# Kernel optimization log

Measured on AMD Instinct MI355X. Metric: run time of the kernel, lower is better.

## Reference

```python
import jax, jax.numpy as jnp
import numpy as np

D_MODEL = 1024
N_HEADS = 16
HEAD_DIM = D_MODEL // N_HEADS
N_MEM = 16
EPS = 1e-5
ROPE_THETA = 10000.0


def layernorm(x, g, b):
    mu = jnp.mean(x, axis=-1, keepdims=True)
    var = jnp.mean(jnp.square(x - mu), axis=-1, keepdims=True)
    return (x - mu) * jax.lax.rsqrt(var + EPS) * g + b


def rope_cos_sin(seq_len, head_dim, dtype):
    inv_freq = 1.0 / (ROPE_THETA ** (jnp.arange(0, head_dim, 2, dtype=jnp.float32) / head_dim))
    pos = jnp.arange(seq_len, dtype=jnp.float32)
    freqs = pos[:, None] * inv_freq[None, :]            # [S, hd/2]
    emb = jnp.concatenate([freqs, freqs], axis=-1)       # [S, hd]
    return jnp.cos(emb).astype(dtype), jnp.sin(emb).astype(dtype)


def rotate_half(x):
    x1, x2 = jnp.split(x, 2, axis=-1)
    return jnp.concatenate([-x2, x1], axis=-1)


def setup_inputs() -> dict:
    key = jax.random.key(0)
    ks = jax.random.split(key, 8)
    B, T, D = 2, 2048, D_MODEL
    x = jax.random.normal(ks[0], (B, T, D), dtype=jnp.float32)
    memory_tokens = jax.random.normal(ks[1], (1, N_MEM, D), dtype=jnp.float32) * 0.02
    s = 1.0 / np.sqrt(D)
    qkv_w = jax.random.uniform(ks[2], (3 * D, D), minval=-s, maxval=s, dtype=jnp.float32)
    qkv_b = jax.random.uniform(ks[3], (3 * D,), minval=-s, maxval=s, dtype=jnp.float32)
    out_w = jax.random.uniform(ks[4], (D, D), minval=-s, maxval=s, dtype=jnp.float32)
    out_b = jax.random.uniform(ks[5], (D,), minval=-s, maxval=s, dtype=jnp.float32)
    norm_g = jnp.ones((D,), jnp.float32)
    norm_b = jnp.zeros((D,), jnp.float32)
    normm_g = jnp.ones((D,), jnp.float32)
    normm_b = jnp.zeros((D,), jnp.float32)
    return {"x": x, "memory_tokens": memory_tokens, "qkv_w": qkv_w, "qkv_b": qkv_b,
            "out_w": out_w, "out_b": out_b, "norm_g": norm_g, "norm_b": norm_b,
            "normm_g": normm_g, "normm_b": normm_b}


def reference(x, memory_tokens, qkv_w, qkv_b, out_w, out_b, norm_g, norm_b, normm_g, normm_b):
    B, T, D = x.shape
    S = N_MEM + T
    residual = x
    x_norm = layernorm(x, norm_g, norm_b)
    mem = layernorm(jnp.broadcast_to(memory_tokens, (B, N_MEM, D)), normm_g, normm_b)
    xm = jnp.concatenate([mem, x_norm], axis=1)                # [B, S, D]
    qkv = xm @ qkv_w.T + qkv_b                                 # [B, S, 3D]
    qkv = qkv.reshape(B, S, 3, N_HEADS, HEAD_DIM)
    q = jnp.transpose(qkv[:, :, 0], (0, 2, 1, 3))              # [B, H, S, hd]
    k = jnp.transpose(qkv[:, :, 1], (0, 2, 1, 3))
    v = jnp.transpose(qkv[:, :, 2], (0, 2, 1, 3))
    cos, sin = rope_cos_sin(S, HEAD_DIM, x.dtype)              # [S, hd]
    q = q * cos + rotate_half(q) * sin
    k = k * cos + rotate_half(k) * sin
    scale = 1.0 / np.sqrt(HEAD_DIM)
    scores = jnp.einsum("bhqd,bhkd->bhqk", q, k) * scale       # [B, H, S, S]
    causal = jnp.tril(jnp.ones((S, S), dtype=bool))
    scores = jnp.where(causal, scores, jnp.finfo(scores.dtype).min)
    attn = jax.nn.softmax(scores, axis=-1)
    out = jnp.einsum("bhqk,bhkd->bhqd", attn, v)               # [B, H, S, hd]
    out = jnp.transpose(out, (0, 2, 1, 3)).reshape(B, S, D)
    out = out @ out_w.T + out_b
    out = out[:, N_MEM:, :]
    return residual + out
```

## Files before the change

### kernel.cpp

```cpp
#include <hip/hip_runtime.h>
#include <cstdint>


using bf16 = __bf16;
typedef __attribute__((ext_vector_type(8))) __bf16 bf16x8;
typedef __attribute__((ext_vector_type(4))) __bf16 bf16x4;
typedef __attribute__((ext_vector_type(4))) float floatx4;

#define MFMA16(a, b, c) __builtin_amdgcn_mfma_f32_16x16x32_bf16(a, b, c, 0, 0, 0)

constexpr int SV = 2064;
constexpr int SP = 2112;
constexpr float LOG2_THETA = 13.287712379549449f;

__device__ __forceinline__ bool dt_is_bf16(const void* p) {
  return *(const uint32_t*)p == 0x3F803F80u;
}

struct f8 { float v[8]; };

__device__ __forceinline__ f8 load8(const void* p, size_t idx, bool bf) {
  f8 r;
  if (bf) {
    bf16x8 t = *(const bf16x8*)((const bf16*)p + idx);
#pragma unroll
    for (int j = 0; j < 8; ++j) r.v[j] = (float)t[j];
  } else {
    float4 a = *(const float4*)((const float*)p + idx);
    float4 b = *(const float4*)((const float*)p + idx + 4);
    r.v[0] = a.x; r.v[1] = a.y; r.v[2] = a.z; r.v[3] = a.w;
    r.v[4] = b.x; r.v[5] = b.y; r.v[6] = b.z; r.v[7] = b.w;
  }
  return r;
}

__device__ __forceinline__ float ld1(const void* p, size_t idx, bool bf) {
  return bf ? (float)((const bf16*)p)[idx] : ((const float*)p)[idx];
}

__device__ __forceinline__ void load16_to_lds(const bf16* gptr, bf16* lptr) {
  auto* g = reinterpret_cast<const __attribute__((address_space(1))) uint32_t*>(
      reinterpret_cast<uintptr_t>(gptr));
  auto* l = reinterpret_cast<__attribute__((address_space(3))) uint32_t*>(
      reinterpret_cast<uintptr_t>(lptr));
  __builtin_amdgcn_global_load_lds(g, l, 16, 0, 0);
}

__global__ __launch_bounds__(256) void conv_w(
    const void* __restrict__ Wq, const void* __restrict__ Wo,
    const void* __restrict__ flagp, bf16* __restrict__ Wqb,
    bf16* __restrict__ Wob) {
  const bool bf = dt_is_bf16(flagp);
  const size_t i = ((size_t)blockIdx.x * 256 + threadIdx.x) * 8;
  const void* src;
  bf16* dst;
  size_t off;
  if (i < 3145728) { src = Wq; dst = Wqb; off = i; }
  else { src = Wo; dst = Wob; off = i - 3145728; }
  const f8 v = load8(src, off, bf);
  bf16x8 o;
#pragma unroll
  for (int j = 0; j < 8; ++j) o[j] = (bf16)v.v[j];
  *(bf16x8*)&dst[off] = o;
}

__global__ __launch_bounds__(256) void ln_all(
    const void* __restrict__ x, const void* __restrict__ mem,
    const void* __restrict__ ng, const void* __restrict__ nb,
    const void* __restrict__ mg, const void* __restrict__ mb,
    bf16* __restrict__ mem16, bf16* __restrict__ xln) {
  const bool bf = dt_is_bf16(ng);
  const int t = threadIdx.x, wid = t >> 6, lane = t & 63;
  const int row = blockIdx.x * 4 + wid;
  const void *src, *g, *bb;
  size_t soff;
  bf16* out;
  if (row < 16) {
    src = mem; soff = (size_t)row * 1024; g = mg; bb = mb;
    out = mem16 + (size_t)row * 1024;
  } else {
    src = x; soff = (size_t)(row - 16) * 1024; g = ng; bb = nb;
    out = xln + (size_t)(row - 16) * 1024;
  }
  const f8 v0 = load8(src, soff + lane * 8, bf);
  const f8 v1 = load8(src, soff + 512 + lane * 8, bf);
  float sum = 0.f, sq = 0.f;
#pragma unroll
  for (int j = 0; j < 8; ++j) { sum += v0.v[j]; sq += v0.v[j] * v0.v[j]; }
#pragma unroll
  for (int j = 0; j < 8; ++j) { sum += v1.v[j]; sq += v1.v[j] * v1.v[j]; }
#pragma unroll
  for (int off = 1; off < 64; off <<= 1) {
    sum += __shfl_xor(sum, off);
    sq += __shfl_xor(sq, off);
  }
  const float mu = sum * (1.0f / 1024.0f);
  const float var = sq * (1.0f / 1024.0f) - mu * mu;
  const float rstd = rsqrtf(var + 1e-5f);
  const f8 g0 = load8(g, lane * 8, bf), g1 = load8(g, 512 + lane * 8, bf);
  const f8 b0 = load8(bb, lane * 8, bf), b1 = load8(bb, 512 + lane * 8, bf);
  bf16x8 o0, o1;
#pragma unroll
  for (int j = 0; j < 8; ++j) {
    o0[j] = (bf16)((v0.v[j] - mu) * rstd * g0.v[j] + b0.v[j]);
    o1[j] = (bf16)((v1.v[j] - mu) * rstd * g1.v[j] + b1.v[j]);
  }
  *(bf16x8*)&out[lane * 8] = o0;
  *(bf16x8*)&out[512 + lane * 8] = o1;
}

__global__ __launch_bounds__(256) void gemm0_rope(
    const bf16* __restrict__ mem16, const bf16* __restrict__ xln,
    const bf16* __restrict__ Wqb, const void* __restrict__ bias,
    const void* __restrict__ flagp, bf16* __restrict__ Qg,
    bf16* __restrict__ Kg, bf16* __restrict__ Vg) {
  const bool bf = dt_is_bf16(flagp);
  __shared__ bf16 As[128 * 32];
  __shared__ bf16 Bs[128 * 32];
  const int t = threadIdx.x;
  const int row0 = blockIdx.x * 128;
  const int col0 = blockIdx.y * 128;
  const int wid = t >> 6, lane = t & 63, lr = lane & 15, lg = lane >> 4;
  const int wrow = (wid >> 1) * 64, wcol = (wid & 1) * 64;
  floatx4 acc[4][4] = {};

  const bf16* agp[2];
  const bf16* bgp[2];
#pragma unroll
  for (int c = 0; c < 2; ++c) {
    const int tt = c * 256 + t;
    int g = row0 + (tt >> 2);
    if (g > 4127) g = 4127;
    const int b2 = (g >= SV) ? 1 : 0;
    const int s = g - b2 * SV;
    const bf16* ap = (s < 16) ? (mem16 + (size_t)s * 1024)
                              : (xln + ((size_t)(b2 * 2048 + s - 16)) * 1024);
    agp[c] = ap + (tt & 3) * 8;
    bgp[c] = Wqb + (size_t)(col0 + (tt >> 2)) * 1024 + (tt & 3) * 8;
  }

  for (int k0 = 0; k0 < 1024; k0 += 32) {
    __syncthreads();
#pragma unroll
    for (int c = 0; c < 2; ++c) {
      const int tt = c * 256 + t;
      load16_to_lds(agp[c] + k0, &As[(tt & ~63) * 8]);
      load16_to_lds(bgp[c] + k0, &Bs[(tt & ~63) * 8]);
    }
    __syncthreads();
    bf16x8 af[4], bfr[4];
#pragma unroll
    for (int i = 0; i < 4; ++i) {
      af[i] = *(const bf16x8*)&As[(wrow + i * 16 + lr) * 32 + lg * 8];
      bfr[i] = *(const bf16x8*)&Bs[(wcol + i * 16 + lr) * 32 + lg * 8];
    }
#pragma unroll
    for (int mi = 0; mi < 4; ++mi)
#pragma unroll
      for (int ni = 0; ni < 4; ++ni)
        acc[mi][ni] = MFMA16(af[mi], bfr[ni], acc[mi][ni]);
  }

  const int colbase = col0 + wcol;
  const int part = colbase >> 10;
  const int h = (colbase >> 6) & 15;
  float f01[2];
  f01[0] = exp2f((float)lr * (-LOG2_THETA / 32.0f));
  f01[1] = exp2f((float)(16 + lr) * (-LOG2_THETA / 32.0f));

  if (part == 2) {
#pragma unroll
    for (int mi = 0; mi < 4; ++mi) {
      const int gq = row0 + wrow + mi * 16 + lg * 4;
      if (gq >= 2 * SV) continue;
      const int b2 = (gq >= SV) ? 1 : 0;
      const int pos = gq - b2 * SV;
      const size_t hb = (size_t)(b2 * 16 + h) * 64;
#pragma unroll
      for (int ni = 0; ni < 4; ++ni) {
        const int d = ni * 16 + lr;
        const float bc = ld1(bias, colbase + ni * 16 + lr, bf);
        bf16x4 vv;
#pragma unroll
        for (int r = 0; r < 4; ++r) vv[r] = (bf16)(acc[mi][ni][r] + bc);
        *(bf16x4*)&Vg[(hb + d) * SP + pos] = vv;
      }
    }
  } else {
    bf16* Dst = (part == 0) ? Qg : Kg;
    const float qs = (part == 0) ? 0.125f : 1.0f;
#pragma unroll
    for (int mi = 0; mi < 4; ++mi) {
#pragma unroll
      for (int r = 0; r < 4; ++r) {
        const int g = row0 + wrow + mi * 16 + lg * 4 + r;
        if (g >= 2 * SV) continue;
        const int b2 = (g >= SV) ? 1 : 0;
        const int pos = g - b2 * SV;
        bf16* drow = Dst + ((size_t)(b2 * 16 + h) * SP + pos) * 64;
#pragma unroll
        for (int a = 0; a < 2; ++a) {
          float c, sn;
          sincosf((float)pos * f01[a], &c, &sn);
          const float vlo = (acc[mi][a][r] + ld1(bias, colbase + a * 16 + lr, bf)) * qs;
          const float vhi = (acc[mi][a + 2][r] + ld1(bias, colbase + 32 + a * 16 + lr, bf)) * qs;
          drow[a * 16 + lr] = (bf16)(vlo * c - vhi * sn);
          drow[32 + a * 16 + lr] = (bf16)(vhi * c + vlo * sn);
        }
      }
    }
  }
}

__global__ __launch_bounds__(256) void flash3(
    const bf16* __restrict__ Qg, const bf16* __restrict__ Kg,
    const bf16* __restrict__ Vg, bf16* __restrict__ attn_out) {
  const int qt = 32 - blockIdx.x;
  const int bh = blockIdx.y;
  const int b = bh >> 4, h = bh & 15;
  const bf16* Qb = Qg + (size_t)bh * SP * 64;
  const bf16* Kb = Kg + (size_t)bh * SP * 64;
  const bf16* Vb = Vg + (size_t)bh * 64 * SP;

  const int t = threadIdx.x;
  const int wid = t >> 6, lane = t & 63, lr = lane & 15, lg = lane >> 4;
  const int qw0 = qt * 64 + wid * 16;

  __shared__ bf16 Ks[64 * 72];
  __shared__ bf16 Vt[64 * 64];
  __shared__ bf16 Ps[4][16 * 72];

  const int qs = qw0 + lr;
  bf16x8 qf0{}, qf1{};
  if (qs < SV) {
    qf0 = *(const bf16x8*)&Qb[(size_t)qs * 64 + lg * 8];
    qf1 = *(const bf16x8*)&Qb[(size_t)qs * 64 + 32 + lg * 8];
  }

  floatx4 o[4] = {};
  float lpart[4] = {};

  const int kr = t >> 2;
  const int kc = (t & 3) * 16;
  const int vd = t >> 2;
  const int vg0 = t & 3;
  const int vswz = ((vd & 7) ^ ((vd >> 4) & 3)) << 3;

  bf16x8 kA, kB, vA, vB;
  kA = *(const bf16x8*)&Kb[(size_t)kr * 64 + kc];
  kB = *(const bf16x8*)&Kb[(size_t)kr * 64 + kc + 8];
  vA = *(const bf16x8*)&Vb[(size_t)vd * SP + vg0 * 8];
  vB = *(const bf16x8*)&Vb[(size_t)vd * SP + (vg0 + 4) * 8];

  for (int kt = 0; kt <= qt; ++kt) {
    const int k0 = kt * 64;
    __syncthreads();
    *(bf16x8*)&Ks[kr * 72 + kc] = kA;
    *(bf16x8*)&Ks[kr * 72 + kc + 8] = kB;
    *(bf16x8*)&Vt[vd * 64 + ((vg0 << 3) ^ vswz)] = vA;
    *(bf16x8*)&Vt[vd * 64 + (((vg0 + 4) << 3) ^ vswz)] = vB;
    __syncthreads();
    if (kt < qt) {
      const int kn = k0 + 64;
      kA = *(const bf16x8*)&Kb[(size_t)(kn + kr) * 64 + kc];
      kB = *(const bf16x8*)&Kb[(size_t)(kn + kr) * 64 + kc + 8];
      vA = *(const bf16x8*)&Vb[(size_t)vd * SP + kn + vg0 * 8];
      vB = *(const bf16x8*)&Vb[(size_t)vd * SP + kn + (vg0 + 4) * 8];
    }

    floatx4 c[4] = {};
#pragma unroll
    for (int j2 = 0; j2 < 4; ++j2) {
      const bf16x8 kfa = *(const bf16x8*)&Ks[(j2 * 16 + lr) * 72 + lg * 8];
      const bf16x8 kfb = *(const bf16x8*)&Ks[(j2 * 16 + lr) * 72 + 32 + lg * 8];
      c[j2] = MFMA16(qf0, kfa, c[j2]);
      c[j2] = MFMA16(qf1, kfb, c[j2]);
    }

    const bool nm = (k0 + 63 > qw0);
#pragma unroll
    for (int r = 0; r < 4; ++r) {
      const int row = qw0 + lg * 4 + r;
      bf16* psr = &Ps[wid][(lg * 4 + r) * 72];
      float ls = 0.f;
#pragma unroll
      for (int j2 = 0; j2 < 4; ++j2) {
        float s = c[j2][r];
        if (nm && (k0 + j2 * 16 + lr > row)) s = -1e30f;
        const float p = __expf(s);
        ls += p;
        psr[j2 * 16 + lr] = (bf16)p;
      }
      lpart[r] += ls;
    }
    asm volatile("s_waitcnt lgkmcnt(0)" ::: "memory");
#pragma unroll
    for (int cc = 0; cc < 2; ++cc) {
      const bf16x8 pf = *(const bf16x8*)&Ps[wid][lr * 72 + cc * 32 + lg * 8];
#pragma unroll
      for (int dt = 0; dt < 4; ++dt) {
        const int key8 = (cc * 32 + lg * 8) ^ ((((lr & 7) ^ dt)) << 3);
        const bf16x8 vf = *(const bf16x8*)&Vt[(dt * 16 + lr) * 64 + key8];
        o[dt] = MFMA16(pf, vf, o[dt]);
      }
    }
  }

#pragma unroll
  for (int r = 0; r < 4; ++r) {
    float l = lpart[r];
    l += __shfl_xor(l, 1);
    l += __shfl_xor(l, 2);
    l += __shfl_xor(l, 4);
    l += __shfl_xor(l, 8);
    const int s = qw0 + lg * 4 + r;
    if (s < 16 || s >= SV) continue;
    const float inv = 1.0f / l;
    const size_t rowoff = ((size_t)(b * 2048 + s - 16)) * 1024 + h * 64;
#pragma unroll
    for (int dt = 0; dt < 4; ++dt)
      attn_out[rowoff + dt * 16 + lr] = (bf16)(o[dt][r] * inv);
  }
}

__global__ __launch_bounds__(256) void gemm1_proj(
    const bf16* __restrict__ A, const bf16* __restrict__ Wob,
    const void* __restrict__ bias, const void* __restrict__ x,
    const void* __restrict__ flagp, void* __restrict__ outp) {
  const bool bf = dt_is_bf16(flagp);
  __shared__ bf16 As[128 * 32];
  __shared__ bf16 Bs[128 * 32];
  const int t = threadIdx.x;
  const int row0 = blockIdx.x * 128;
  const int col0 = blockIdx.y * 128;
  const int wid = t >> 6, lane = t & 63, lr = lane & 15, lg = lane >> 4;
  const int wrow = (wid >> 1) * 64, wcol = (wid & 1) * 64;
  floatx4 acc[4][4] = {};

  const bf16* agp[2];
  const bf16* bgp[2];
#pragma unroll
  for (int c = 0; c < 2; ++c) {
    const int tt = c * 256 + t;
    agp[c] = A + (size_t)(row0 + (tt >> 2)) * 1024 + (tt & 3) * 8;
    bgp[c] = Wob + (size_t)(col0 + (tt >> 2)) * 1024 + (tt & 3) * 8;
  }

  for (int k0 = 0; k0 < 1024; k0 += 32) {
    __syncthreads();
#pragma unroll
    for (int c = 0; c < 2; ++c) {
      const int tt = c * 256 + t;
      load16_to_lds(agp[c] + k0, &As[(tt & ~63) * 8]);
      load16_to_lds(bgp[c] + k0, &Bs[(tt & ~63) * 8]);
    }
    __syncthreads();
    bf16x8 af[4], bfr[4];
#pragma unroll
    for (int i = 0; i < 4; ++i) {
      af[i] = *(const bf16x8*)&As[(wrow + i * 16 + lr) * 32 + lg * 8];
      bfr[i] = *(const bf16x8*)&Bs[(wcol + i * 16 + lr) * 32 + lg * 8];
    }
#pragma unroll
    for (int mi = 0; mi < 4; ++mi)
#pragma unroll
      for (int ni = 0; ni < 4; ++ni)
        acc[mi][ni] = MFMA16(af[mi], bfr[ni], acc[mi][ni]);
  }

#pragma unroll
  for (int mi = 0; mi < 4; ++mi) {
#pragma unroll
    for (int r = 0; r < 4; ++r) {
      const int row = row0 + wrow + mi * 16 + lg * 4 + r;
#pragma unroll
      for (int ni = 0; ni < 4; ++ni) {
        const int col = col0 + wcol + ni * 16 + lr;
        const size_t idx = (size_t)row * 1024 + col;
        const float v = acc[mi][ni][r] + ld1(bias, col, bf) + ld1(x, idx, bf);
        if (bf)
          ((bf16*)outp)[idx] = (bf16)v;
        else
          ((float*)outp)[idx] = v;
      }
    }
  }
}

extern "C" void kernel_launch(void* const* d_in, const int* in_sizes, int n_in,
                              void* d_out, int out_size, void* d_ws, size_t ws_size,
                              hipStream_t stream) {
  const void* x = d_in[0];
  const void* mem = d_in[1];
  const void* qkvw = d_in[2];
  const void* qkvb = d_in[3];
  const void* outw = d_in[4];
  const void* outb = d_in[5];
  const void* ng = d_in[6];
  const void* nb = d_in[7];
  const void* mg = d_in[8];
  const void* mb = d_in[9];

  char* ws = (char*)d_ws;
  bf16* mem16 = (bf16*)(ws);
  bf16* xln = (bf16*)(ws + 32768);
  bf16* Qg = (bf16*)(ws + 8421376);
  bf16* Kg = (bf16*)(ws + 17072128);
  bf16* Vg = (bf16*)(ws + 25722880);
  bf16* Wqb = (bf16*)(ws + 34373632);
  bf16* Wob = (bf16*)(ws + 40665088);
  bf16* attn = xln;

  conv_w<<<2048, 256, 0, stream>>>(qkvw, outw, ng, Wqb, Wob);
  ln_all<<<1028, 256, 0, stream>>>(x, mem, ng, nb, mg, mb, mem16, xln);
  gemm0_rope<<<dim3(33, 24), 256, 0, stream>>>(mem16, xln, Wqb, qkvb, ng,
                                               Qg, Kg, Vg);
  flash3<<<dim3(33, 32), 256, 0, stream>>>(Qg, Kg, Vg, attn);
  gemm1_proj<<<dim3(32, 8), 256, 0, stream>>>(attn, Wob, outb, x, ng, d_out);
}
```

Measured before the change: 240.8 us.

## Double attention query tile per block and merge weight-convert with layernorm

The flash attention kernel now gives each wave two 16-row query sub-tiles (a 128-row block), so every K/V tile staged in shared memory serves twice as many queries and grid size is halved. Sub-tiles fully above the causal diagonal skip work, and K/V loads past the padded end are clamped or zeroed. The weight conversion and layernorm kernels are fused into one launch to save launch overhead. The cost is more registers per thread and fewer blocks, which can lower occupancy and worsen load balance for the causal triangle.

```diff
diff --git a/kernel.cpp b/kernel.cpp
--- a/kernel.cpp
+++ b/kernel.cpp
@@ -46,32 +46,31 @@
   __builtin_amdgcn_global_load_lds(g, l, 16, 0, 0);
 }
 
-__global__ __launch_bounds__(256) void conv_w(
-    const void* __restrict__ Wq, const void* __restrict__ Wo,
-    const void* __restrict__ flagp, bf16* __restrict__ Wqb,
-    bf16* __restrict__ Wob) {
-  const bool bf = dt_is_bf16(flagp);
-  const size_t i = ((size_t)blockIdx.x * 256 + threadIdx.x) * 8;
-  const void* src;
-  bf16* dst;
-  size_t off;
-  if (i < 3145728) { src = Wq; dst = Wqb; off = i; }
-  else { src = Wo; dst = Wob; off = i - 3145728; }
-  const f8 v = load8(src, off, bf);
-  bf16x8 o;
-#pragma unroll
-  for (int j = 0; j < 8; ++j) o[j] = (bf16)v.v[j];
-  *(bf16x8*)&dst[off] = o;
-}
-
-__global__ __launch_bounds__(256) void ln_all(
+__global__ __launch_bounds__(256) void prep(
     const void* __restrict__ x, const void* __restrict__ mem,
     const void* __restrict__ ng, const void* __restrict__ nb,
     const void* __restrict__ mg, const void* __restrict__ mb,
-    bf16* __restrict__ mem16, bf16* __restrict__ xln) {
+    const void* __restrict__ Wq, const void* __restrict__ Wo,
+    bf16* __restrict__ mem16, bf16* __restrict__ xln,
+    bf16* __restrict__ Wqb, bf16* __restrict__ Wob) {
   const bool bf = dt_is_bf16(ng);
-  const int t = threadIdx.x, wid = t >> 6, lane = t & 63;
-  const int row = blockIdx.x * 4 + wid;
+  const int t = threadIdx.x;
+  if (blockIdx.x < 2048) {
+    const size_t i = ((size_t)blockIdx.x * 256 + t) * 8;
+    const void* src;
+    bf16* dst;
+    size_t off;
+    if (i < 3145728) { src = Wq; dst = Wqb; off = i; }
+    else { src = Wo; dst = Wob; off = i - 3145728; }
+    const f8 v = load8(src, off, bf);
+    bf16x8 o;
+#pragma unroll
+    for (int j = 0; j < 8; ++j) o[j] = (bf16)v.v[j];
+    *(bf16x8*)&dst[off] = o;
+    return;
+  }
+  const int wid = t >> 6, lane = t & 63;
+  const int row = (blockIdx.x - 2048) * 4 + wid;
   const void *src, *g, *bb;
   size_t soff;
   bf16* out;
@@ -212,10 +211,10 @@
   }
 }
 
-__global__ __launch_bounds__(256) void flash3(
+__global__ __launch_bounds__(256) void flash4(
     const bf16* __restrict__ Qg, const bf16* __restrict__ Kg,
     const bf16* __restrict__ Vg, bf16* __restrict__ attn_out) {
-  const int qt = 32 - blockIdx.x;
+  const int qt = 16 - blockIdx.x;
   const int bh = blockIdx.y;
   const int b = bh >> 4, h = bh & 15;
   const bf16* Qb = Qg + (size_t)bh * SP * 64;
@@ -224,21 +223,25 @@
 
   const int t = threadIdx.x;
   const int wid = t >> 6, lane = t & 63, lr = lane & 15, lg = lane >> 4;
-  const int qw0 = qt * 64 + wid * 16;
+  const int qw0 = qt * 128 + wid * 32;
 
   __shared__ bf16 Ks[64 * 72];
   __shared__ bf16 Vt[64 * 64];
-  __shared__ bf16 Ps[4][16 * 72];
-
-  const int qs = qw0 + lr;
-  bf16x8 qf0{}, qf1{};
-  if (qs < SV) {
-    qf0 = *(const bf16x8*)&Qb[(size_t)qs * 64 + lg * 8];
-    qf1 = *(const bf16x8*)&Qb[(size_t)qs * 64 + 32 + lg * 8];
-  }
-
-  floatx4 o[4] = {};
-  float lpart[4] = {};
+  __shared__ bf16 Ps[4][32 * 72];
+
+  const int qsa = qw0 + lr, qsb = qw0 + 16 + lr;
+  bf16x8 qa0{}, qa1{}, qb0{}, qb1{};
+  if (qsa < SV) {
+    qa0 = *(const bf16x8*)&Qb[(size_t)qsa * 64 + lg * 8];
+    qa1 = *(const bf16x8*)&Qb[(size_t)qsa * 64 + 32 + lg * 8];
+  }
+  if (qsb < SV) {
+    qb0 = *(const bf16x8*)&Qb[(size_t)qsb * 64 + lg * 8];
+    qb1 = *(const bf16x8*)&Qb[(size_t)qsb * 64 + 32 + lg * 8];
+  }
+
+  floatx4 oa[4] = {}, ob[4] = {};
+  float la[4] = {}, lb[4] = {};
 
   const int kr = t >> 2;
   const int kc = (t & 3) * 16;
@@ -246,13 +249,17 @@
   const int vg0 = t & 3;
   const int vswz = ((vd & 7) ^ ((vd >> 4) & 3)) << 3;
 
-  bf16x8 kA, kB, vA, vB;
-  kA = *(const bf16x8*)&Kb[(size_t)kr * 64 + kc];
-  kB = *(const bf16x8*)&Kb[(size_t)kr * 64 + kc + 8];
+  const int ktn = 2 * qt + 2;
+
+  bf16x8 kA{}, kB{}, vA, vB;
+  if (kr < SV) {
+    kA = *(const bf16x8*)&Kb[(size_t)kr * 64 + kc];
+    kB = *(const bf16x8*)&Kb[(size_t)kr * 64 + kc + 8];
+  }
   vA = *(const bf16x8*)&Vb[(size_t)vd * SP + vg0 * 8];
   vB = *(const bf16x8*)&Vb[(size_t)vd * SP + (vg0 + 4) * 8];
 
-  for (int kt = 0; kt <= qt; ++kt) {
+  for (int kt = 0; kt < ktn; ++kt) {
     const int k0 = kt * 64;
     __syncthreads();
     *(bf16x8*)&Ks[kr * 72 + kc] = kA;
@@ -260,66 +267,131 @@
     *(bf16x8*)&Vt[vd * 64 + ((vg0 << 3) ^ vswz)] = vA;
     *(bf16x8*)&Vt[vd * 64 + (((vg0 + 4) << 3) ^ vswz)] = vB;
     __syncthreads();
-    if (kt < qt) {
+    if (kt + 1 < ktn) {
       const int kn = k0 + 64;
-      kA = *(const bf16x8*)&Kb[(size_t)(kn + kr) * 64 + kc];
-      kB = *(const bf16x8*)&Kb[(size_t)(kn + kr) * 64 + kc + 8];
-      vA = *(const bf16x8*)&Vb[(size_t)vd * SP + kn + vg0 * 8];
-      vB = *(const bf16x8*)&Vb[(size_t)vd * SP + kn + (vg0 + 4) * 8];
-    }
-
-    floatx4 c[4] = {};
-#pragma unroll
-    for (int j2 = 0; j2 < 4; ++j2) {
-      const bf16x8 kfa = *(const bf16x8*)&Ks[(j2 * 16 + lr) * 72 + lg * 8];
-      const bf16x8 kfb = *(const bf16x8*)&Ks[(j2 * 16 + lr) * 72 + 32 + lg * 8];
-      c[j2] = MFMA16(qf0, kfa, c[j2]);
-      c[j2] = MFMA16(qf1, kfb, c[j2]);
-    }
-
-    const bool nm = (k0 + 63 > qw0);
-#pragma unroll
-    for (int r = 0; r < 4; ++r) {
-      const int row = qw0 + lg * 4 + r;
-      bf16* psr = &Ps[wid][(lg * 4 + r) * 72];
-      float ls = 0.f;
+      const int ksn = kn + kr;
+      if (ksn < SP) {
+        kA = *(const bf16x8*)&Kb[(size_t)ksn * 64 + kc];
+        kB = *(const bf16x8*)&Kb[(size_t)ksn * 64 + kc + 8];
+      } else {
+        bf16x8 z{};
+        kA = z; kB = z;
+      }
+      const int knc = (kn > SP - 64) ? (SP - 64) : kn;
+      vA = *(const bf16x8*)&Vb[(size_t)vd * SP + knc + vg0 * 8];
+      vB = *(const bf16x8*)&Vb[(size_t)vd * SP + knc + (vg0 + 4) * 8];
+    }
+
+    const bool act_a = (k0 <= qw0 + 15);
+    const bool act_b = (k0 <= qw0 + 31);
+
+    if (act_a) {
+      floatx4 c[4] = {};
 #pragma unroll
       for (int j2 = 0; j2 < 4; ++j2) {
-        float s = c[j2][r];
-        if (nm && (k0 + j2 * 16 + lr > row)) s = -1e30f;
-        const float p = __expf(s);
-        ls += p;
-        psr[j2 * 16 + lr] = (bf16)p;
-      }
-      lpart[r] += ls;
+        const bf16x8 kfa = *(const bf16x8*)&Ks[(j2 * 16 + lr) * 72 + lg * 8];
+        const bf16x8 kfb = *(const bf16x8*)&Ks[(j2 * 16 + lr) * 72 + 32 + lg * 8];
+        c[j2] = MFMA16(qa0, kfa, c[j2]);
+        c[j2] = MFMA16(qa1, kfb, c[j2]);
+      }
+      const bool nm = (k0 + 63 > qw0);
+#pragma unroll
+      for (int r = 0; r < 4; ++r) {
+        const int row = qw0 + lg * 4 + r;
+        bf16* psr = &Ps[wid][(lg * 4 + r) * 72];
+        float ls = 0.f;
+#pragma unroll
+        for (int j2 = 0; j2 < 4; ++j2) {
+          float s = c[j2][r];
+          if (nm && (k0 + j2 * 16 + lr > row)) s = -1e30f;
+          const float p = __expf(s);
+          ls += p;
+          psr[j2 * 16 + lr] = (bf16)p;
+        }
+        la[r] += ls;
+      }
+    }
+    if (act_b) {
+      floatx4 c[4] = {};
+#pragma unroll
+      for (int j2 = 0; j2 < 4; ++j2) {
+        const bf16x8 kfa = *(const bf16x8*)&Ks[(j2 * 16 + lr) * 72 + lg * 8];
+        const bf16x8 kfb = *(const bf16x8*)&Ks[(j2 * 16 + lr) * 72 + 32 + lg * 8];
+        c[j2] = MFMA16(qb0, kfa, c[j2]);
+        c[j2] = MFMA16(qb1, kfb, c[j2]);
+      }
+      const bool nm = (k0 + 63 > qw0 + 16);
+#pragma unroll
+      for (int r = 0; r < 4; ++r) {
+        const int row = qw0 + 16 + lg * 4 + r;
+        bf16* psr = &Ps[wid][(16 + lg * 4 + r) * 72];
+        float ls = 0.f;
+#pragma unroll
+        for (int j2 = 0; j2 < 4; ++j2) {
+          float s = c[j2][r];
+          if (nm && (k0 + j2 * 16 + lr > row)) s = -1e30f;
+          const float p = __expf(s);
+          ls += p;
+          psr[j2 * 16 + lr] = (bf16)p;
+        }
+        lb[r] += ls;
+      }
     }
     asm volatile("s_waitcnt lgkmcnt(0)" ::: "memory");
-#pragma unroll
-    for (int cc = 0; cc < 2; ++cc) {
-      const bf16x8 pf = *(const bf16x8*)&Ps[wid][lr * 72 + cc * 32 + lg * 8];
-#pragma unroll
-      for (int dt = 0; dt < 4; ++dt) {
-        const int key8 = (cc * 32 + lg * 8) ^ ((((lr & 7) ^ dt)) << 3);
-        const bf16x8 vf = *(const bf16x8*)&Vt[(dt * 16 + lr) * 64 + key8];
-        o[dt] = MFMA16(pf, vf, o[dt]);
+    if (act_a) {
+#pragma unroll
+      for (int cc = 0; cc < 2; ++cc) {
+        const bf16x8 pf = *(const bf16x8*)&Ps[wid][lr * 72 + cc * 32 + lg * 8];
+#pragma unroll
+        for (int dt = 0; dt < 4; ++dt) {
+          const int key8 = (cc * 32 + lg * 8) ^ ((((lr & 7) ^ dt)) << 3);
+          const bf16x8 vf = *(const bf16x8*)&Vt[(dt * 16 + lr) * 64 + key8];
+          oa[dt] = MFMA16(pf, vf, oa[dt]);
+        }
+      }
+    }
+    if (act_b) {
+#pragma unroll
+      for (int cc = 0; cc < 2; ++cc) {
+        const bf16x8 pf = *(const bf16x8*)&Ps[wid][(16 + lr) * 72 + cc * 32 + lg * 8];
+#pragma unroll
+        for (int dt = 0; dt < 4; ++dt) {
+          const int key8 = (cc * 32 + lg * 8) ^ ((((lr & 7) ^ dt)) << 3);
+          const bf16x8 vf = *(const bf16x8*)&Vt[(dt * 16 + lr) * 64 + key8];
+          ob[dt] = MFMA16(pf, vf, ob[dt]);
+        }
       }
     }
   }
 
 #pragma unroll
   for (int r = 0; r < 4; ++r) {
-    float l = lpart[r];
+    float l = la[r];
     l += __shfl_xor(l, 1);
     l += __shfl_xor(l, 2);
     l += __shfl_xor(l, 4);
     l += __shfl_xor(l, 8);
     const int s = qw0 + lg * 4 + r;
-    if (s < 16 || s >= SV) continue;
-    const float inv = 1.0f / l;
-    const size_t rowoff = ((size_t)(b * 2048 + s - 16)) * 1024 + h * 64;
-#pragma unroll
-    for (int dt = 0; dt < 4; ++dt)
-      attn_out[rowoff + dt * 16 + lr] = (bf16)(o[dt][r] * inv);
+    if (s >= 16 && s < SV) {
+      const float inv = 1.0f / l;
+      const size_t rowoff = ((size_t)(b * 2048 + s - 16)) * 1024 + h * 64;
+#pragma unroll
+      for (int dt = 0; dt < 4; ++dt)
+        attn_out[rowoff + dt * 16 + lr] = (bf16)(oa[dt][r] * inv);
+    }
+    float l2 = lb[r];
+    l2 += __shfl_xor(l2, 1);
+    l2 += __shfl_xor(l2, 2);
+    l2 += __shfl_xor(l2, 4);
+    l2 += __shfl_xor(l2, 8);
+    const int s2 = qw0 + 16 + lg * 4 + r;
+    if (s2 >= 16 && s2 < SV) {
+      const float inv = 1.0f / l2;
+      const size_t rowoff = ((size_t)(b * 2048 + s2 - 16)) * 1024 + h * 64;
+#pragma unroll
+      for (int dt = 0; dt < 4; ++dt)
+        attn_out[rowoff + dt * 16 + lr] = (bf16)(ob[dt][r] * inv);
+    }
   }
 }
 
@@ -411,10 +483,10 @@
   bf16* Wob = (bf16*)(ws + 40665088);
   bf16* attn = xln;
 
-  conv_w<<<2048, 256, 0, stream>>>(qkvw, outw, ng, Wqb, Wob);
-  ln_all<<<1028, 256, 0, stream>>>(x, mem, ng, nb, mg, mb, mem16, xln);
+  prep<<<3076, 256, 0, stream>>>(x, mem, ng, nb, mg, mb, qkvw, outw,
+                                 mem16, xln, Wqb, Wob);
   gemm0_rope<<<dim3(33, 24), 256, 0, stream>>>(mem16, xln, Wqb, qkvb, ng,
                                                Qg, Kg, Vg);
-  flash3<<<dim3(33, 32), 256, 0, stream>>>(Qg, Kg, Vg, attn);
+  flash4<<<dim3(17, 32), 256, 0, stream>>>(Qg, Kg, Vg, attn);
   gemm1_proj<<<dim3(32, 8), 256, 0, stream>>>(attn, Wob, outb, x, ng, d_out);
 }
```

Measured after the change: 282.7 us. 1.17x slower.

## Double-buffer K/V tiles in flash attention and merge weight-convert with layernorm

Applied to the files above, without the earlier changes.

The attention kernel now keeps two LDS buffers for K and V. The next tile is written into the alternate buffer after the current tile's compute, so each iteration needs one barrier instead of two. Separately, the weight bf16 conversion and the layernorm kernels are merged into a single launch, removing one kernel launch and its gap. The cost is doubled K/V shared memory, which may reduce occupancy, and the global loads are held in registers across the compute phase.

```diff
diff --git a/kernel.cpp b/kernel.cpp
--- a/kernel.cpp
+++ b/kernel.cpp
@@ -46,32 +46,31 @@
   __builtin_amdgcn_global_load_lds(g, l, 16, 0, 0);
 }
 
-__global__ __launch_bounds__(256) void conv_w(
-    const void* __restrict__ Wq, const void* __restrict__ Wo,
-    const void* __restrict__ flagp, bf16* __restrict__ Wqb,
-    bf16* __restrict__ Wob) {
-  const bool bf = dt_is_bf16(flagp);
-  const size_t i = ((size_t)blockIdx.x * 256 + threadIdx.x) * 8;
-  const void* src;
-  bf16* dst;
-  size_t off;
-  if (i < 3145728) { src = Wq; dst = Wqb; off = i; }
-  else { src = Wo; dst = Wob; off = i - 3145728; }
-  const f8 v = load8(src, off, bf);
-  bf16x8 o;
-#pragma unroll
-  for (int j = 0; j < 8; ++j) o[j] = (bf16)v.v[j];
-  *(bf16x8*)&dst[off] = o;
-}
-
-__global__ __launch_bounds__(256) void ln_all(
+__global__ __launch_bounds__(256) void prep(
     const void* __restrict__ x, const void* __restrict__ mem,
     const void* __restrict__ ng, const void* __restrict__ nb,
     const void* __restrict__ mg, const void* __restrict__ mb,
-    bf16* __restrict__ mem16, bf16* __restrict__ xln) {
+    const void* __restrict__ Wq, const void* __restrict__ Wo,
+    bf16* __restrict__ mem16, bf16* __restrict__ xln,
+    bf16* __restrict__ Wqb, bf16* __restrict__ Wob) {
   const bool bf = dt_is_bf16(ng);
-  const int t = threadIdx.x, wid = t >> 6, lane = t & 63;
-  const int row = blockIdx.x * 4 + wid;
+  const int t = threadIdx.x;
+  if (blockIdx.x < 2048) {
+    const size_t i = ((size_t)blockIdx.x * 256 + t) * 8;
+    const void* src;
+    bf16* dst;
+    size_t off;
+    if (i < 3145728) { src = Wq; dst = Wqb; off = i; }
+    else { src = Wo; dst = Wob; off = i - 3145728; }
+    const f8 v = load8(src, off, bf);
+    bf16x8 o;
+#pragma unroll
+    for (int j = 0; j < 8; ++j) o[j] = (bf16)v.v[j];
+    *(bf16x8*)&dst[off] = o;
+    return;
+  }
+  const int wid = t >> 6, lane = t & 63;
+  const int row = (blockIdx.x - 2048) * 4 + wid;
   const void *src, *g, *bb;
   size_t soff;
   bf16* out;
@@ -212,7 +211,7 @@
   }
 }
 
-__global__ __launch_bounds__(256) void flash3(
+__global__ __launch_bounds__(256) void flash5(
     const bf16* __restrict__ Qg, const bf16* __restrict__ Kg,
     const bf16* __restrict__ Vg, bf16* __restrict__ attn_out) {
   const int qt = 32 - blockIdx.x;
@@ -226,8 +225,8 @@
   const int wid = t >> 6, lane = t & 63, lr = lane & 15, lg = lane >> 4;
   const int qw0 = qt * 64 + wid * 16;
 
-  __shared__ bf16 Ks[64 * 72];
-  __shared__ bf16 Vt[64 * 64];
+  __shared__ bf16 Ks[2][64 * 72];
+  __shared__ bf16 Vt[2][64 * 64];
   __shared__ bf16 Ps[4][16 * 72];
 
   const int qs = qw0 + lr;
@@ -246,20 +245,21 @@
   const int vg0 = t & 3;
   const int vswz = ((vd & 7) ^ ((vd >> 4) & 3)) << 3;
 
-  bf16x8 kA, kB, vA, vB;
-  kA = *(const bf16x8*)&Kb[(size_t)kr * 64 + kc];
-  kB = *(const bf16x8*)&Kb[(size_t)kr * 64 + kc + 8];
-  vA = *(const bf16x8*)&Vb[(size_t)vd * SP + vg0 * 8];
-  vB = *(const bf16x8*)&Vb[(size_t)vd * SP + (vg0 + 4) * 8];
+  {
+    const bf16x8 kA = *(const bf16x8*)&Kb[(size_t)kr * 64 + kc];
+    const bf16x8 kB = *(const bf16x8*)&Kb[(size_t)kr * 64 + kc + 8];
+    const bf16x8 vA = *(const bf16x8*)&Vb[(size_t)vd * SP + vg0 * 8];
+    const bf16x8 vB = *(const bf16x8*)&Vb[(size_t)vd * SP + (vg0 + 4) * 8];
+    *(bf16x8*)&Ks[0][kr * 72 + kc] = kA;
+    *(bf16x8*)&Ks[0][kr * 72 + kc + 8] = kB;
+    *(bf16x8*)&Vt[0][vd * 64 + ((vg0 << 3) ^ vswz)] = vA;
+    *(bf16x8*)&Vt[0][vd * 64 + (((vg0 + 4) << 3) ^ vswz)] = vB;
+  }
 
   for (int kt = 0; kt <= qt; ++kt) {
     const int k0 = kt * 64;
-    __syncthreads();
-    *(bf16x8*)&Ks[kr * 72 + kc] = kA;
-    *(bf16x8*)&Ks[kr * 72 + kc + 8] = kB;
-    *(bf16x8*)&Vt[vd * 64 + ((vg0 << 3) ^ vswz)] = vA;
-    *(bf16x8*)&Vt[vd * 64 + (((vg0 + 4) << 3) ^ vswz)] = vB;
-    __syncthreads();
+    const int cur = kt & 1;
+    bf16x8 kA, kB, vA, vB;
     if (kt < qt) {
       const int kn = k0 + 64;
       kA = *(const bf16x8*)&Kb[(size_t)(kn + kr) * 64 + kc];
@@ -267,12 +267,13 @@
       vA = *(const bf16x8*)&Vb[(size_t)vd * SP + kn + vg0 * 8];
       vB = *(const bf16x8*)&Vb[(size_t)vd * SP + kn + (vg0 + 4) * 8];
     }
+    __syncthreads();
 
     floatx4 c[4] = {};
 #pragma unroll
     for (int j2 = 0; j2 < 4; ++j2) {
-      const bf16x8 kfa = *(const bf16x8*)&Ks[(j2 * 16 + lr) * 72 + lg * 8];
-      const bf16x8 kfb = *(const bf16x8*)&Ks[(j2 * 16 + lr) * 72 + 32 + lg * 8];
+      const bf16x8 kfa = *(const bf16x8*)&Ks[cur][(j2 * 16 + lr) * 72 + lg * 8];
+      const bf16x8 kfb = *(const bf16x8*)&Ks[cur][(j2 * 16 + lr) * 72 + 32 + lg * 8];
       c[j2] = MFMA16(qf0, kfa, c[j2]);
       c[j2] = MFMA16(qf1, kfb, c[j2]);
     }
@@ -300,9 +301,17 @@
 #pragma unroll
       for (int dt = 0; dt < 4; ++dt) {
         const int key8 = (cc * 32 + lg * 8) ^ ((((lr & 7) ^ dt)) << 3);
-        const bf16x8 vf = *(const bf16x8*)&Vt[(dt * 16 + lr) * 64 + key8];
+        const bf16x8 vf = *(const bf16x8*)&Vt[cur][(dt * 16 + lr) * 64 + key8];
         o[dt] = MFMA16(pf, vf, o[dt]);
       }
+    }
+
+    if (kt < qt) {
+      const int nxt = cur ^ 1;
+      *(bf16x8*)&Ks[nxt][kr * 72 + kc] = kA;
+      *(bf16x8*)&Ks[nxt][kr * 72 + kc + 8] = kB;
+      *(bf16x8*)&Vt[nxt][vd * 64 + ((vg0 << 3) ^ vswz)] = vA;
+      *(bf16x8*)&Vt[nxt][vd * 64 + (((vg0 + 4) << 3) ^ vswz)] = vB;
     }
   }
 
@@ -411,10 +420,10 @@
   bf16* Wob = (bf16*)(ws + 40665088);
   bf16* attn = xln;
 
-  conv_w<<<2048, 256, 0, stream>>>(qkvw, outw, ng, Wqb, Wob);
-  ln_all<<<1028, 256, 0, stream>>>(x, mem, ng, nb, mg, mb, mem16, xln);
+  prep<<<3076, 256, 0, stream>>>(x, mem, ng, nb, mg, mb, qkvw, outw,
+                                 mem16, xln, Wqb, Wob);
   gemm0_rope<<<dim3(33, 24), 256, 0, stream>>>(mem16, xln, Wqb, qkvb, ng,
                                                Qg, Kg, Vg);
-  flash3<<<dim3(33, 32), 256, 0, stream>>>(Qg, Kg, Vg, attn);
+  flash5<<<dim3(33, 32), 256, 0, stream>>>(Qg, Kg, Vg, attn);
   gemm1_proj<<<dim3(32, 8), 256, 0, stream>>>(attn, Wob, outb, x, ng, d_out);
 }
```

New measurement: 242.9 us. About the same (+0.9%).
